# Kernel tuning notes

Hardware: AMD Instinct MI355X
Metric: run time of the kernel (lower is better)

The kernel has to match this reference:

```python
import jax, jax.numpy as jnp
import numpy as np

B, C_IN, L, NCLASS = 256, 6, 512, 10

def setup_inputs() -> dict:
    key = jax.random.key(0)
    ks = jax.random.split(key, 16)
    g = lambda k, shp, s=0.05: jax.random.normal(k, shp, dtype=jnp.float32) * s
    return {
        "x": jax.random.normal(ks[0], (B, C_IN, L), dtype=jnp.float32),
        "conv1_w": g(ks[1], (32, C_IN, 3)),
        "conv1_b": g(ks[2], (32,)),
        "bn1_g": jnp.ones((32,), jnp.float32),
        "bn1_b": jnp.zeros((32,), jnp.float32),
        "bn1_m": g(ks[3], (32,)),
        "bn1_v": jnp.abs(g(ks[4], (32,))) + 1.0,
        "conv2_w": g(ks[5], (64, 32, 3)),
        "conv2_b": g(ks[6], (64,)),
        "bn2_g": jnp.ones((64,), jnp.float32),
        "bn2_b": jnp.zeros((64,), jnp.float32),
        "bn2_m": g(ks[7], (64,)),
        "bn2_v": jnp.abs(g(ks[8], (64,))) + 1.0,
        "wq": g(ks[9], (64, 64)),
        "bq": g(ks[10], (64,)),
        "wk": g(ks[11], (64, 64)),
        "bk": g(ks[12], (64,)),
        "wv": g(ks[13], (64, 64)),
        "bv": g(ks[14], (64,)),
        "fc_w": g(ks[15], (NCLASS, 64)),
        "fc_b": jnp.zeros((NCLASS,), jnp.float32),
    }

def _conv1d(x, w, b):
    # x: [B, C, L], w: [O, C, 3], padding=1 -> same length
    y = jax.lax.conv_general_dilated(
        x, w, window_strides=(1,), padding=[(1, 1)],
        dimension_numbers=("NCH", "OIH", "NCH"))
    return y + b[None, :, None]

def _bn(x, g, b, m, v, eps=1e-5):
    # eval-mode BatchNorm1d over channel dim of [B, C, L]
    inv = g * jax.lax.rsqrt(v + eps)
    return x * inv[None, :, None] + (b - m * inv)[None, :, None]

def reference(x, conv1_w, conv1_b, bn1_g, bn1_b, bn1_m, bn1_v,
              conv2_w, conv2_b, bn2_g, bn2_b, bn2_m, bn2_v,
              wq, bq, wk, bk, wv, bv, fc_w, fc_b):
    h = jax.nn.relu(_bn(_conv1d(x, conv1_w, conv1_b), bn1_g, bn1_b, bn1_m, bn1_v))
    h = jax.nn.relu(_bn(_conv1d(h, conv2_w, conv2_b), bn2_g, bn2_b, bn2_m, bn2_v))
    h = h.transpose(0, 2, 1)                      # [B, L, 64]
    q = h @ wq.T + bq
    k = h @ wk.T + bk
    v = h @ wv.T + bv
    scores = jnp.einsum("bqd,bkd->bqk", q, k) / jnp.sqrt(jnp.float32(64.0))
    attn = jax.nn.softmax(scores, axis=-1)
    out = jnp.einsum("bqk,bkd->bqd", attn, v)     # [B, L, 64]
    pooled = out.mean(axis=1)                     # [B, 64]
    return pooled @ fc_w.T + fc_b                 # [B, n_class]
```

## Files before the change

kernel.cpp:

```cpp
#include <hip/hip_runtime.h>
#include <hip/hip_bf16.h>


#define NB 256
#define LL 512
#define CIN 6
#define NCLASS 10
#define SLAB 8192
#define QSC 0.18033688f

typedef __bf16 bf16x8 __attribute__((ext_vector_type(8)));
typedef float f32x4 __attribute__((ext_vector_type(4)));
typedef unsigned short us4 __attribute__((ext_vector_type(4)));
typedef unsigned short us8 __attribute__((ext_vector_type(8)));
typedef unsigned int u32x4 __attribute__((ext_vector_type(4)));

static __device__ __forceinline__ unsigned short f2b(float f) {
    __bf16 h = (__bf16)f;
    return __builtin_bit_cast(unsigned short, h);
}

__global__ __launch_bounds__(256) void prep_weights(
    const float* __restrict__ w1, const float* __restrict__ cb1,
    const float* __restrict__ g1, const float* __restrict__ be1,
    const float* __restrict__ m1, const float* __restrict__ v1,
    const float* __restrict__ w2, const float* __restrict__ cb2,
    const float* __restrict__ g2, const float* __restrict__ be2,
    const float* __restrict__ m2, const float* __restrict__ v2,
    const float* __restrict__ wq, const float* __restrict__ wk,
    const float* __restrict__ wv,
    unsigned short* __restrict__ w1p, float* __restrict__ b1f,
    unsigned short* __restrict__ w2p, float* __restrict__ b2f,
    unsigned short* __restrict__ wqp, unsigned short* __restrict__ wkp,
    unsigned short* __restrict__ wvp)
{
    const int tt = blockIdx.x * 256 + threadIdx.x;
    for (int idx = tt; idx < 1024; idx += 2048) {
        int c = idx >> 5, k = idx & 31;
        int dl = k >> 3, ci = k & 7;
        float inv = g1[c] * rsqrtf(v1[c] + 1e-5f);
        float val = (dl < 3 && ci < 6) ? w1[c * 18 + ci * 3 + dl] * inv : 0.f;
        w1p[idx] = f2b(val);
    }
    if (tt < 32) {
        float inv = g1[tt] * rsqrtf(v1[tt] + 1e-5f);
        b1f[tt] = be1[tt] + (cb1[tt] - m1[tt]) * inv;
    }
    for (int idx = tt; idx < 2048; idx += 2048) {
        int c2 = idx >> 5, ci = idx & 31;
        float inv = g2[c2] * rsqrtf(v2[c2] + 1e-5f);
        const float* wp = w2 + c2 * 96 + ci * 3;
        w2p[c2 * 96 +      ci] = f2b(wp[0] * inv);
        w2p[c2 * 96 + 32 + ci] = f2b(wp[1] * inv);
        w2p[c2 * 96 + 64 + ci] = f2b(wp[2] * inv);
    }
    if (tt >= 64 && tt < 128) {
        int c2 = tt - 64;
        float inv = g2[c2] * rsqrtf(v2[c2] + 1e-5f);
        b2f[c2] = be2[c2] + (cb2[c2] - m2[c2]) * inv;
    }
    for (int idx = tt; idx < 4096; idx += 2048) {
        int d = idx >> 6, k = idx & 63;
        int kc = k >> 5, quad = (k >> 3) & 3, e = k & 7;
        int ch = kc * 32 + (e >> 2) * 16 + quad * 4 + (e & 3);
        wqp[idx] = f2b(wq[d * 64 + ch] * QSC);
        wkp[idx] = f2b(wk[d * 64 + ch]);
        wvp[idx] = f2b(wv[d * 64 + ch]);
    }
}

__global__ __launch_bounds__(512, 2) void fused_all(
    const float* __restrict__ x,
    const unsigned short* __restrict__ w1p, const float* __restrict__ b1f,
    const unsigned short* __restrict__ w2p, const float* __restrict__ b2f,
    const unsigned short* __restrict__ wqp, const unsigned short* __restrict__ wkp,
    const unsigned short* __restrict__ wvp,
    const float* __restrict__ bq, const float* __restrict__ bk,
    const float* __restrict__ bvp,
    const float* __restrict__ fcw, const float* __restrict__ fcb,
    float* __restrict__ outp)
{
    const int b = blockIdx.x;
    const int t = threadIdx.x;
    const int w = t >> 6, lane = t & 63, quad = lane >> 4, lc = lane & 15;

    __shared__ __align__(16) char smem[16 * SLAB + 8192];
    unsigned short* xstage = (unsigned short*)(smem + 16 * SLAB);
    float* redw   = (float*)(smem + 16 * SLAB) + w * 64;
    float* pooled = (float*)(smem + 16 * SLAB + 4096);

    {
        us8 pk;
        #pragma unroll
        for (int ci = 0; ci < 6; ci++)
            pk[ci] = f2b(x[((size_t)b * CIN + ci) * LL + t]);
        pk[6] = 0; pk[7] = 0;
        *(us8*)&xstage[t * 8] = pk;
    }
    __syncthreads();

    bf16x8 aQ4[4][2];
    #pragma unroll
    for (int sg = 0; sg < 2; sg++) {
        const int g = 2 * w + sg;
        char* gslab = smem + g * SLAB;
        unsigned short* h1sl = (unsigned short*)gslab;
        unsigned short* Kf   = (unsigned short*)gslab;
        unsigned short* Vf   = (unsigned short*)(gslab + 4096);

        bf16x8 bW1[2];
        #pragma unroll
        for (int nt = 0; nt < 2; nt++)
            bW1[nt] = *(const bf16x8*)(w1p + (nt * 16 + lc) * 32 + quad * 8);
        f32x4 b1q[2];
        #pragma unroll
        for (int nt = 0; nt < 2; nt++)
            b1q[nt] = *(const f32x4*)&b1f[nt * 16 + quad * 4];
        #pragma unroll
        for (int mt = 0; mt < 3; mt++) {
            int j = mt * 16 + lc;
            int P = g * 32 - 1 + j;
            int src = P + quad - 1;
            bool okx = (src >= 0) && (src < LL);
            int srcc = src < 0 ? 0 : (src > 511 ? 511 : src);
            u32x4 xv = *(const u32x4*)&xstage[srcc * 8];
            if (!okx) { xv[0] = 0u; xv[1] = 0u; xv[2] = 0u; xv[3] = 0u; }
            bf16x8 aX = __builtin_bit_cast(bf16x8, xv);
            bool pv = (P >= 0) && (P < LL);
            #pragma unroll
            for (int nt = 0; nt < 2; nt++) {
                f32x4 z = {0.f, 0.f, 0.f, 0.f};
                f32x4 h = __builtin_amdgcn_mfma_f32_16x16x32_bf16(bW1[nt], aX, z, 0, 0, 0);
                us4 pk;
                #pragma unroll
                for (int r = 0; r < 4; r++) {
                    float y = h[r] + b1q[nt][r];
                    y = (pv && y > 0.f) ? y : 0.f;
                    pk[r] = f2b(y);
                }
                if (j < 34)
                    *(us4*)&h1sl[j * 40 + nt * 16 + quad * 4] = pk;
            }
        }

        bf16x8 bX[2][3], aW2[4][3];
        #pragma unroll
        for (int rt = 0; rt < 2; rt++)
            #pragma unroll
            for (int kc = 0; kc < 3; kc++)
                bX[rt][kc] = *(const bf16x8*)&h1sl[(rt * 16 + lc + kc) * 40 + quad * 8];
        #pragma unroll
        for (int nt = 0; nt < 4; nt++)
            #pragma unroll
            for (int kc = 0; kc < 3; kc++)
                aW2[nt][kc] = *(const bf16x8*)(w2p + (nt * 16 + lc) * 96 + kc * 32 + quad * 8);

        f32x4 acc2[4][2];
        #pragma unroll
        for (int nt = 0; nt < 4; nt++)
            #pragma unroll
            for (int rt = 0; rt < 2; rt++) {
                f32x4 a = {0.f, 0.f, 0.f, 0.f};
                a = __builtin_amdgcn_mfma_f32_16x16x32_bf16(aW2[nt][0], bX[rt][0], a, 0, 0, 0);
                a = __builtin_amdgcn_mfma_f32_16x16x32_bf16(aW2[nt][1], bX[rt][1], a, 0, 0, 0);
                acc2[nt][rt] = __builtin_amdgcn_mfma_f32_16x16x32_bf16(aW2[nt][2], bX[rt][2], a, 0, 0, 0);
            }

        bf16x8 aH[2][2];
        #pragma unroll
        for (int nt2 = 0; nt2 < 4; nt2++) {
            f32x4 bb2 = *(const f32x4*)&b2f[nt2 * 16 + quad * 4];
            #pragma unroll
            for (int rt = 0; rt < 2; rt++)
                #pragma unroll
                for (int reg = 0; reg < 4; reg++) {
                    float y = acc2[nt2][rt][reg] + bb2[reg];
                    aH[rt][nt2 >> 1][(nt2 & 1) * 4 + reg] = (__bf16)(y > 0.f ? y : 0.f);
                }
        }

        {
            f32x4 Cq[4][2], bbq[4];
            #pragma unroll
            for (int nt = 0; nt < 4; nt++) {
                bf16x8 aW0 = *(const bf16x8*)(wqp + (nt * 16 + lc) * 64 + quad * 8);
                bf16x8 aW1 = *(const bf16x8*)(wqp + (nt * 16 + lc) * 64 + 32 + quad * 8);
                bbq[nt] = *(const f32x4*)&bq[nt * 16 + quad * 4];
                #pragma unroll
                for (int rt = 0; rt < 2; rt++) {
                    f32x4 a = {0.f, 0.f, 0.f, 0.f};
                    a = __builtin_amdgcn_mfma_f32_16x16x32_bf16(aW0, aH[rt][0], a, 0, 0, 0);
                    Cq[nt][rt] = __builtin_amdgcn_mfma_f32_16x16x32_bf16(aW1, aH[rt][1], a, 0, 0, 0);
                }
            }
            #pragma unroll
            for (int rt = 0; rt < 2; rt++)
                #pragma unroll
                for (int nt = 0; nt < 4; nt++)
                    #pragma unroll
                    for (int reg = 0; reg < 4; reg++)
                        aQ4[sg * 2 + rt][nt >> 1][(nt & 1) * 4 + reg] =
                            (__bf16)(Cq[nt][rt][reg] + bbq[nt][reg] * QSC);
        }
        {
            f32x4 Ck[4][2], bbk[4];
            #pragma unroll
            for (int nt = 0; nt < 4; nt++) {
                bf16x8 aW0 = *(const bf16x8*)(wkp + (nt * 16 + lc) * 64 + quad * 8);
                bf16x8 aW1 = *(const bf16x8*)(wkp + (nt * 16 + lc) * 64 + 32 + quad * 8);
                bbk[nt] = *(const f32x4*)&bk[nt * 16 + quad * 4];
                #pragma unroll
                for (int rt = 0; rt < 2; rt++) {
                    f32x4 a = {0.f, 0.f, 0.f, 0.f};
                    a = __builtin_amdgcn_mfma_f32_16x16x32_bf16(aW0, aH[rt][0], a, 0, 0, 0);
                    Ck[nt][rt] = __builtin_amdgcn_mfma_f32_16x16x32_bf16(aW1, aH[rt][1], a, 0, 0, 0);
                }
            }
            #pragma unroll
            for (int rt = 0; rt < 2; rt++)
                #pragma unroll
                for (int kc = 0; kc < 2; kc++) {
                    us8 pk;
                    #pragma unroll
                    for (int e = 0; e < 8; e++) {
                        int nt = kc * 2 + (e >> 2), reg = e & 3;
                        pk[e] = f2b(Ck[nt][rt][reg] + bbk[nt][reg]);
                    }
                    *(us8*)&Kf[((rt * 2 + kc) << 9) + lane * 8] = pk;
                }
        }

        #pragma unroll
        for (int nt = 0; nt < 4; nt++) {
            bf16x8 bW0 = *(const bf16x8*)(wvp + (nt * 16 + lc) * 64 + quad * 8);
            bf16x8 bW1 = *(const bf16x8*)(wvp + (nt * 16 + lc) * 64 + 32 + quad * 8);
            const float bvv = bvp[nt * 16 + lc];
            f32x4 a0, a1;
            {
                f32x4 z = {0.f, 0.f, 0.f, 0.f};
                z = __builtin_amdgcn_mfma_f32_16x16x32_bf16(aH[0][0], bW0, z, 0, 0, 0);
                a0 = __builtin_amdgcn_mfma_f32_16x16x32_bf16(aH[0][1], bW1, z, 0, 0, 0);
            }
            {
                f32x4 z = {0.f, 0.f, 0.f, 0.f};
                z = __builtin_amdgcn_mfma_f32_16x16x32_bf16(aH[1][0], bW0, z, 0, 0, 0);
                a1 = __builtin_amdgcn_mfma_f32_16x16x32_bf16(aH[1][1], bW1, z, 0, 0, 0);
            }
            us8 pk;
            #pragma unroll
            for (int reg = 0; reg < 4; reg++) {
                pk[reg]     = f2b(a0[reg] + bvv);
                pk[4 + reg] = f2b(a1[reg] + bvv);
            }
            *(us8*)&Vf[nt * 512 + lane * 8] = pk;
        }
    }

    __syncthreads();

    f32x4 outacc[4][4];
    #pragma unroll
    for (int rt = 0; rt < 4; rt++)
        #pragma unroll
        for (int dt = 0; dt < 4; dt++) outacc[rt][dt] = (f32x4){0.f, 0.f, 0.f, 0.f};
    float den[4] = {0.f, 0.f, 0.f, 0.f};

    bf16x8 bK2[2][2];
    {
        const unsigned short* sK = (const unsigned short*)smem;
        #pragma unroll
        for (int nt = 0; nt < 2; nt++)
            #pragma unroll
            for (int kc = 0; kc < 2; kc++)
                bK2[nt][kc] = *(const bf16x8*)&sK[((nt * 2 + kc) << 9) + lane * 8];
    }
    f32x4 sv[2][4];
    #pragma unroll
    for (int nt = 0; nt < 2; nt++)
        #pragma unroll
        for (int rt = 0; rt < 4; rt++) {
            f32x4 z = {0.f, 0.f, 0.f, 0.f};
            z = __builtin_amdgcn_mfma_f32_16x16x32_bf16(bK2[nt][0], aQ4[rt][0], z, 0, 0, 0);
            sv[nt][rt] = __builtin_amdgcn_mfma_f32_16x16x32_bf16(bK2[nt][1], aQ4[rt][1], z, 0, 0, 0);
        }

    for (int cc = 0; cc < 16; cc++) {
        const unsigned short* sV = (const unsigned short*)(smem + cc * SLAB + 4096);
        bf16x8 bV[4];
        #pragma unroll
        for (int dt = 0; dt < 4; dt++)
            bV[dt] = *(const bf16x8*)&sV[dt * 512 + lane * 8];
        if (cc < 15) {
            const unsigned short* sKn = (const unsigned short*)(smem + (cc + 1) * SLAB);
            #pragma unroll
            for (int nt = 0; nt < 2; nt++)
                #pragma unroll
                for (int kc = 0; kc < 2; kc++)
                    bK2[nt][kc] = *(const bf16x8*)&sKn[((nt * 2 + kc) << 9) + lane * 8];
        }
        bf16x8 aP[4];
        #pragma unroll
        for (int rt = 0; rt < 4; rt++)
            #pragma unroll
            for (int nt = 0; nt < 2; nt++)
                #pragma unroll
                for (int reg = 0; reg < 4; reg++) {
                    float p = __builtin_amdgcn_exp2f(sv[nt][rt][reg]);
                    den[rt] += p;
                    aP[rt][nt * 4 + reg] = (__bf16)p;
                }
        __builtin_amdgcn_s_setprio(1);
        #pragma unroll
        for (int rt = 0; rt < 4; rt++)
            #pragma unroll
            for (int dt = 0; dt < 4; dt++)
                outacc[rt][dt] = __builtin_amdgcn_mfma_f32_16x16x32_bf16(aP[rt], bV[dt], outacc[rt][dt], 0, 0, 0);
        if (cc < 15) {
            #pragma unroll
            for (int nt = 0; nt < 2; nt++)
                #pragma unroll
                for (int rt = 0; rt < 4; rt++) {
                    f32x4 z = {0.f, 0.f, 0.f, 0.f};
                    z = __builtin_amdgcn_mfma_f32_16x16x32_bf16(bK2[nt][0], aQ4[rt][0], z, 0, 0, 0);
                    sv[nt][rt] = __builtin_amdgcn_mfma_f32_16x16x32_bf16(bK2[nt][1], aQ4[rt][1], z, 0, 0, 0);
                }
        }
        __builtin_amdgcn_s_setprio(0);
    }

    float rden[4][4];
    #pragma unroll
    for (int rt = 0; rt < 4; rt++) {
        float d2 = den[rt];
        d2 += __shfl_xor(d2, 16);
        d2 += __shfl_xor(d2, 32);
        d2 = 1.0f / d2;
        #pragma unroll
        for (int reg = 0; reg < 4; reg++)
            rden[rt][reg] = __shfl(d2, quad * 4 + reg);
    }
    #pragma unroll
    for (int dt = 0; dt < 4; dt++) {
        float ps = 0.f;
        #pragma unroll
        for (int rt = 0; rt < 4; rt++)
            #pragma unroll
            for (int reg = 0; reg < 4; reg++)
                ps += outacc[rt][dt][reg] * rden[rt][reg];
        ps += __shfl_xor(ps, 16);
        ps += __shfl_xor(ps, 32);
        if (quad == 0) redw[dt * 16 + lc] = ps;
    }
    __syncthreads();
    if (t < 64) {
        float s = 0.f;
        #pragma unroll
        for (int ww = 0; ww < 8; ww++)
            s += *(const float*)(smem + 16 * SLAB + ww * 256 + t * 4);
        pooled[t] = s * (1.0f / 512.0f);
    }
    __syncthreads();
    if (t < NCLASS) {
        float acc = fcb[t];
        #pragma unroll
        for (int d = 0; d < 64; d++) acc += pooled[d] * fcw[t * 64 + d];
        outp[b * NCLASS + t] = acc;
    }
}

extern "C" void kernel_launch(void* const* d_in, const int* in_sizes, int n_in,
                              void* d_out, int out_size, void* d_ws, size_t ws_size,
                              hipStream_t stream)
{
    const float* x   = (const float*)d_in[0];
    const float* w1  = (const float*)d_in[1];
    const float* cb1 = (const float*)d_in[2];
    const float* g1  = (const float*)d_in[3];
    const float* be1 = (const float*)d_in[4];
    const float* m1  = (const float*)d_in[5];
    const float* v1  = (const float*)d_in[6];
    const float* w2  = (const float*)d_in[7];
    const float* cb2 = (const float*)d_in[8];
    const float* g2  = (const float*)d_in[9];
    const float* be2 = (const float*)d_in[10];
    const float* m2  = (const float*)d_in[11];
    const float* v2  = (const float*)d_in[12];
    const float* wq  = (const float*)d_in[13];
    const float* bq  = (const float*)d_in[14];
    const float* wk  = (const float*)d_in[15];
    const float* bk  = (const float*)d_in[16];
    const float* wv  = (const float*)d_in[17];
    const float* bv  = (const float*)d_in[18];
    const float* fcw = (const float*)d_in[19];
    const float* fcb = (const float*)d_in[20];
    float* out = (float*)d_out;

    char* ws = (char*)d_ws;
    unsigned short* w1p = (unsigned short*)(ws);
    float*          b1f = (float*)(ws + 2048u);
    float*          b2f = (float*)(ws + 2176u);
    unsigned short* w2p = (unsigned short*)(ws + 2432u);
    unsigned short* wqp = (unsigned short*)(ws + 14720u);
    unsigned short* wkp = (unsigned short*)(ws + 22912u);
    unsigned short* wvp = (unsigned short*)(ws + 31104u);

    prep_weights<<<dim3(8), 256, 0, stream>>>(w1, cb1, g1, be1, m1, v1,
                                              w2, cb2, g2, be2, m2, v2,
                                              wq, wk, wv,
                                              w1p, b1f, w2p, b2f, wqp, wkp, wvp);
    fused_all<<<dim3(NB), 512, 0, stream>>>(x, w1p, b1f, w2p, b2f,
                                            wqp, wkp, wvp,
                                            bq, bk, bv, fcw, fcb, out);
}
```

Measured before the change: 124.2 us.

## Batch both slab groups per wave and compute softmax denominator via MFMA

Restructures the per-wave prologue so conv2 and the Q/K/V projections for both slab groups run in one pass, loading each weight fragment once and reusing it across both groups instead of reloading it per group. In the attention loop, the softmax denominator is now an extra MFMA against a vector of ones, replacing per-element float adds and the later cross-lane shuffle reduction. This moves VALU work onto the matrix unit but adds MFMA instructions, raises register pressure from the doubled live arrays, and sums the denominator over bf16-rounded probabilities instead of fp32 ones.

```diff
diff --git a/kernel.cpp b/kernel.cpp
--- a/kernel.cpp
+++ b/kernel.cpp
@@ -89,6 +89,9 @@
     float* redw   = (float*)(smem + 16 * SLAB) + w * 64;
     float* pooled = (float*)(smem + 16 * SLAB + 4096);
 
+    unsigned short* slab[2] = { (unsigned short*)(smem + (2 * w) * SLAB),
+                                (unsigned short*)(smem + (2 * w + 1) * SLAB) };
+
     {
         us8 pk;
         #pragma unroll
@@ -99,15 +102,7 @@
     }
     __syncthreads();
 
-    bf16x8 aQ4[4][2];
-    #pragma unroll
-    for (int sg = 0; sg < 2; sg++) {
-        const int g = 2 * w + sg;
-        char* gslab = smem + g * SLAB;
-        unsigned short* h1sl = (unsigned short*)gslab;
-        unsigned short* Kf   = (unsigned short*)gslab;
-        unsigned short* Vf   = (unsigned short*)(gslab + 4096);
-
+    {
         bf16x8 bW1[2];
         #pragma unroll
         for (int nt = 0; nt < 2; nt++)
@@ -117,134 +112,153 @@
         for (int nt = 0; nt < 2; nt++)
             b1q[nt] = *(const f32x4*)&b1f[nt * 16 + quad * 4];
         #pragma unroll
-        for (int mt = 0; mt < 3; mt++) {
-            int j = mt * 16 + lc;
-            int P = g * 32 - 1 + j;
-            int src = P + quad - 1;
-            bool okx = (src >= 0) && (src < LL);
-            int srcc = src < 0 ? 0 : (src > 511 ? 511 : src);
-            u32x4 xv = *(const u32x4*)&xstage[srcc * 8];
-            if (!okx) { xv[0] = 0u; xv[1] = 0u; xv[2] = 0u; xv[3] = 0u; }
-            bf16x8 aX = __builtin_bit_cast(bf16x8, xv);
-            bool pv = (P >= 0) && (P < LL);
-            #pragma unroll
-            for (int nt = 0; nt < 2; nt++) {
-                f32x4 z = {0.f, 0.f, 0.f, 0.f};
-                f32x4 h = __builtin_amdgcn_mfma_f32_16x16x32_bf16(bW1[nt], aX, z, 0, 0, 0);
-                us4 pk;
-                #pragma unroll
-                for (int r = 0; r < 4; r++) {
-                    float y = h[r] + b1q[nt][r];
-                    y = (pv && y > 0.f) ? y : 0.f;
-                    pk[r] = f2b(y);
+        for (int sg = 0; sg < 2; sg++) {
+            const int g = 2 * w + sg;
+            unsigned short* h1sl = slab[sg];
+            #pragma unroll
+            for (int mt = 0; mt < 3; mt++) {
+                int j = mt * 16 + lc;
+                int P = g * 32 - 1 + j;
+                int src = P + quad - 1;
+                bool okx = (src >= 0) && (src < LL);
+                int srcc = src < 0 ? 0 : (src > 511 ? 511 : src);
+                u32x4 xv = *(const u32x4*)&xstage[srcc * 8];
+                if (!okx) { xv[0] = 0u; xv[1] = 0u; xv[2] = 0u; xv[3] = 0u; }
+                bf16x8 aX = __builtin_bit_cast(bf16x8, xv);
+                bool pv = (P >= 0) && (P < LL);
+                #pragma unroll
+                for (int nt = 0; nt < 2; nt++) {
+                    f32x4 z = {0.f, 0.f, 0.f, 0.f};
+                    f32x4 h = __builtin_amdgcn_mfma_f32_16x16x32_bf16(bW1[nt], aX, z, 0, 0, 0);
+                    us4 pk;
+                    #pragma unroll
+                    for (int r = 0; r < 4; r++) {
+                        float y = h[r] + b1q[nt][r];
+                        y = (pv && y > 0.f) ? y : 0.f;
+                        pk[r] = f2b(y);
+                    }
+                    if (j < 34)
+                        *(us4*)&h1sl[j * 40 + nt * 16 + quad * 4] = pk;
                 }
-                if (j < 34)
-                    *(us4*)&h1sl[j * 40 + nt * 16 + quad * 4] = pk;
-            }
-        }
-
-        bf16x8 bX[2][3], aW2[4][3];
+            }
+        }
+    }
+
+    bf16x8 bX[2][2][3];
+    #pragma unroll
+    for (int sg = 0; sg < 2; sg++)
         #pragma unroll
         for (int rt = 0; rt < 2; rt++)
             #pragma unroll
             for (int kc = 0; kc < 3; kc++)
-                bX[rt][kc] = *(const bf16x8*)&h1sl[(rt * 16 + lc + kc) * 40 + quad * 8];
-        #pragma unroll
-        for (int nt = 0; nt < 4; nt++)
-            #pragma unroll
-            for (int kc = 0; kc < 3; kc++)
-                aW2[nt][kc] = *(const bf16x8*)(w2p + (nt * 16 + lc) * 96 + kc * 32 + quad * 8);
-
-        f32x4 acc2[4][2];
-        #pragma unroll
-        for (int nt = 0; nt < 4; nt++)
+                bX[sg][rt][kc] = *(const bf16x8*)&slab[sg][(rt * 16 + lc + kc) * 40 + quad * 8];
+
+    f32x4 acc2[2][4][2];
+    #pragma unroll
+    for (int nt = 0; nt < 4; nt++) {
+        bf16x8 aW0 = *(const bf16x8*)(w2p + (nt * 16 + lc) * 96 + quad * 8);
+        bf16x8 aW1 = *(const bf16x8*)(w2p + (nt * 16 + lc) * 96 + 32 + quad * 8);
+        bf16x8 aW2 = *(const bf16x8*)(w2p + (nt * 16 + lc) * 96 + 64 + quad * 8);
+        #pragma unroll
+        for (int sg = 0; sg < 2; sg++)
             #pragma unroll
             for (int rt = 0; rt < 2; rt++) {
                 f32x4 a = {0.f, 0.f, 0.f, 0.f};
-                a = __builtin_amdgcn_mfma_f32_16x16x32_bf16(aW2[nt][0], bX[rt][0], a, 0, 0, 0);
-                a = __builtin_amdgcn_mfma_f32_16x16x32_bf16(aW2[nt][1], bX[rt][1], a, 0, 0, 0);
-                acc2[nt][rt] = __builtin_amdgcn_mfma_f32_16x16x32_bf16(aW2[nt][2], bX[rt][2], a, 0, 0, 0);
-            }
-
-        bf16x8 aH[2][2];
-        #pragma unroll
-        for (int nt2 = 0; nt2 < 4; nt2++) {
-            f32x4 bb2 = *(const f32x4*)&b2f[nt2 * 16 + quad * 4];
+                a = __builtin_amdgcn_mfma_f32_16x16x32_bf16(aW0, bX[sg][rt][0], a, 0, 0, 0);
+                a = __builtin_amdgcn_mfma_f32_16x16x32_bf16(aW1, bX[sg][rt][1], a, 0, 0, 0);
+                acc2[sg][nt][rt] = __builtin_amdgcn_mfma_f32_16x16x32_bf16(aW2, bX[sg][rt][2], a, 0, 0, 0);
+            }
+    }
+
+    bf16x8 aH[2][2][2];
+    #pragma unroll
+    for (int nt2 = 0; nt2 < 4; nt2++) {
+        f32x4 bb2 = *(const f32x4*)&b2f[nt2 * 16 + quad * 4];
+        #pragma unroll
+        for (int sg = 0; sg < 2; sg++)
             #pragma unroll
             for (int rt = 0; rt < 2; rt++)
                 #pragma unroll
                 for (int reg = 0; reg < 4; reg++) {
-                    float y = acc2[nt2][rt][reg] + bb2[reg];
-                    aH[rt][nt2 >> 1][(nt2 & 1) * 4 + reg] = (__bf16)(y > 0.f ? y : 0.f);
+                    float y = acc2[sg][nt2][rt][reg] + bb2[reg];
+                    aH[sg][rt][nt2 >> 1][(nt2 & 1) * 4 + reg] = (__bf16)(y > 0.f ? y : 0.f);
                 }
-        }
-
-        {
-            f32x4 Cq[4][2], bbq[4];
-            #pragma unroll
-            for (int nt = 0; nt < 4; nt++) {
-                bf16x8 aW0 = *(const bf16x8*)(wqp + (nt * 16 + lc) * 64 + quad * 8);
-                bf16x8 aW1 = *(const bf16x8*)(wqp + (nt * 16 + lc) * 64 + 32 + quad * 8);
-                bbq[nt] = *(const f32x4*)&bq[nt * 16 + quad * 4];
+    }
+
+    f32x4 bbq[4], bbk[4];
+    #pragma unroll
+    for (int nt = 0; nt < 4; nt++) {
+        bbq[nt] = *(const f32x4*)&bq[nt * 16 + quad * 4];
+        bbk[nt] = *(const f32x4*)&bk[nt * 16 + quad * 4];
+    }
+
+    bf16x8 aQ4[4][2];
+    #pragma unroll
+    for (int nt = 0; nt < 4; nt++) {
+        bf16x8 aW0 = *(const bf16x8*)(wqp + (nt * 16 + lc) * 64 + quad * 8);
+        bf16x8 aW1 = *(const bf16x8*)(wqp + (nt * 16 + lc) * 64 + 32 + quad * 8);
+        #pragma unroll
+        for (int sg = 0; sg < 2; sg++)
+            #pragma unroll
+            for (int rt = 0; rt < 2; rt++) {
+                f32x4 a = {0.f, 0.f, 0.f, 0.f};
+                a = __builtin_amdgcn_mfma_f32_16x16x32_bf16(aW0, aH[sg][rt][0], a, 0, 0, 0);
+                a = __builtin_amdgcn_mfma_f32_16x16x32_bf16(aW1, aH[sg][rt][1], a, 0, 0, 0);
+                #pragma unroll
+                for (int reg = 0; reg < 4; reg++)
+                    aQ4[sg * 2 + rt][nt >> 1][(nt & 1) * 4 + reg] =
+                        (__bf16)(a[reg] + bbq[nt][reg] * QSC);
+            }
+    }
+
+    #pragma unroll
+    for (int kc = 0; kc < 2; kc++) {
+        f32x4 Ck[2][2][2];
+        #pragma unroll
+        for (int j = 0; j < 2; j++) {
+            int nt = kc * 2 + j;
+            bf16x8 aW0 = *(const bf16x8*)(wkp + (nt * 16 + lc) * 64 + quad * 8);
+            bf16x8 aW1 = *(const bf16x8*)(wkp + (nt * 16 + lc) * 64 + 32 + quad * 8);
+            #pragma unroll
+            for (int sg = 0; sg < 2; sg++)
                 #pragma unroll
                 for (int rt = 0; rt < 2; rt++) {
                     f32x4 a = {0.f, 0.f, 0.f, 0.f};
-                    a = __builtin_amdgcn_mfma_f32_16x16x32_bf16(aW0, aH[rt][0], a, 0, 0, 0);
-                    Cq[nt][rt] = __builtin_amdgcn_mfma_f32_16x16x32_bf16(aW1, aH[rt][1], a, 0, 0, 0);
+                    a = __builtin_amdgcn_mfma_f32_16x16x32_bf16(aW0, aH[sg][rt][0], a, 0, 0, 0);
+                    Ck[j][sg][rt] = __builtin_amdgcn_mfma_f32_16x16x32_bf16(aW1, aH[sg][rt][1], a, 0, 0, 0);
                 }
-            }
-            #pragma unroll
-            for (int rt = 0; rt < 2; rt++)
-                #pragma unroll
-                for (int nt = 0; nt < 4; nt++)
-                    #pragma unroll
-                    for (int reg = 0; reg < 4; reg++)
-                        aQ4[sg * 2 + rt][nt >> 1][(nt & 1) * 4 + reg] =
-                            (__bf16)(Cq[nt][rt][reg] + bbq[nt][reg] * QSC);
-        }
-        {
-            f32x4 Ck[4][2], bbk[4];
-            #pragma unroll
-            for (int nt = 0; nt < 4; nt++) {
-                bf16x8 aW0 = *(const bf16x8*)(wkp + (nt * 16 + lc) * 64 + quad * 8);
-                bf16x8 aW1 = *(const bf16x8*)(wkp + (nt * 16 + lc) * 64 + 32 + quad * 8);
-                bbk[nt] = *(const f32x4*)&bk[nt * 16 + quad * 4];
-                #pragma unroll
-                for (int rt = 0; rt < 2; rt++) {
-                    f32x4 a = {0.f, 0.f, 0.f, 0.f};
-                    a = __builtin_amdgcn_mfma_f32_16x16x32_bf16(aW0, aH[rt][0], a, 0, 0, 0);
-                    Ck[nt][rt] = __builtin_amdgcn_mfma_f32_16x16x32_bf16(aW1, aH[rt][1], a, 0, 0, 0);
+        }
+        #pragma unroll
+        for (int sg = 0; sg < 2; sg++)
+            #pragma unroll
+            for (int rt = 0; rt < 2; rt++) {
+                us8 pk;
+                #pragma unroll
+                for (int e = 0; e < 8; e++) {
+                    int j = e >> 2, reg = e & 3, nt = kc * 2 + j;
+                    pk[e] = f2b(Ck[j][sg][rt][reg] + bbk[nt][reg]);
                 }
-            }
-            #pragma unroll
-            for (int rt = 0; rt < 2; rt++)
-                #pragma unroll
-                for (int kc = 0; kc < 2; kc++) {
-                    us8 pk;
-                    #pragma unroll
-                    for (int e = 0; e < 8; e++) {
-                        int nt = kc * 2 + (e >> 2), reg = e & 3;
-                        pk[e] = f2b(Ck[nt][rt][reg] + bbk[nt][reg]);
-                    }
-                    *(us8*)&Kf[((rt * 2 + kc) << 9) + lane * 8] = pk;
-                }
-        }
-
-        #pragma unroll
-        for (int nt = 0; nt < 4; nt++) {
-            bf16x8 bW0 = *(const bf16x8*)(wvp + (nt * 16 + lc) * 64 + quad * 8);
-            bf16x8 bW1 = *(const bf16x8*)(wvp + (nt * 16 + lc) * 64 + 32 + quad * 8);
-            const float bvv = bvp[nt * 16 + lc];
+                *(us8*)&slab[sg][((rt * 2 + kc) << 9) + lane * 8] = pk;
+            }
+    }
+
+    #pragma unroll
+    for (int nt = 0; nt < 4; nt++) {
+        bf16x8 bW0 = *(const bf16x8*)(wvp + (nt * 16 + lc) * 64 + quad * 8);
+        bf16x8 bW1 = *(const bf16x8*)(wvp + (nt * 16 + lc) * 64 + 32 + quad * 8);
+        const float bvv = bvp[nt * 16 + lc];
+        #pragma unroll
+        for (int sg = 0; sg < 2; sg++) {
             f32x4 a0, a1;
             {
                 f32x4 z = {0.f, 0.f, 0.f, 0.f};
-                z = __builtin_amdgcn_mfma_f32_16x16x32_bf16(aH[0][0], bW0, z, 0, 0, 0);
-                a0 = __builtin_amdgcn_mfma_f32_16x16x32_bf16(aH[0][1], bW1, z, 0, 0, 0);
+                z = __builtin_amdgcn_mfma_f32_16x16x32_bf16(aH[sg][0][0], bW0, z, 0, 0, 0);
+                a0 = __builtin_amdgcn_mfma_f32_16x16x32_bf16(aH[sg][0][1], bW1, z, 0, 0, 0);
             }
             {
                 f32x4 z = {0.f, 0.f, 0.f, 0.f};
-                z = __builtin_amdgcn_mfma_f32_16x16x32_bf16(aH[1][0], bW0, z, 0, 0, 0);
-                a1 = __builtin_amdgcn_mfma_f32_16x16x32_bf16(aH[1][1], bW1, z, 0, 0, 0);
+                z = __builtin_amdgcn_mfma_f32_16x16x32_bf16(aH[sg][1][0], bW0, z, 0, 0, 0);
+                a1 = __builtin_amdgcn_mfma_f32_16x16x32_bf16(aH[sg][1][1], bW1, z, 0, 0, 0);
             }
             us8 pk;
             #pragma unroll
@@ -252,7 +266,7 @@
                 pk[reg]     = f2b(a0[reg] + bvv);
                 pk[4 + reg] = f2b(a1[reg] + bvv);
             }
-            *(us8*)&Vf[nt * 512 + lane * 8] = pk;
+            *(us8*)&slab[sg][2048 + nt * 512 + lane * 8] = pk;
         }
     }
 
@@ -263,7 +277,12 @@
     for (int rt = 0; rt < 4; rt++)
         #pragma unroll
         for (int dt = 0; dt < 4; dt++) outacc[rt][dt] = (f32x4){0.f, 0.f, 0.f, 0.f};
-    float den[4] = {0.f, 0.f, 0.f, 0.f};
+    f32x4 accDen[4];
+    #pragma unroll
+    for (int rt = 0; rt < 4; rt++) accDen[rt] = (f32x4){0.f, 0.f, 0.f, 0.f};
+    bf16x8 bOne;
+    #pragma unroll
+    for (int e = 0; e < 8; e++) bOne[e] = (__bf16)1.0f;
 
     bf16x8 bK2[2][2];
     {
@@ -304,17 +323,16 @@
             #pragma unroll
             for (int nt = 0; nt < 2; nt++)
                 #pragma unroll
-                for (int reg = 0; reg < 4; reg++) {
-                    float p = __builtin_amdgcn_exp2f(sv[nt][rt][reg]);
-                    den[rt] += p;
-                    aP[rt][nt * 4 + reg] = (__bf16)p;
-                }
+                for (int reg = 0; reg < 4; reg++)
+                    aP[rt][nt * 4 + reg] = (__bf16)__builtin_amdgcn_exp2f(sv[nt][rt][reg]);
         __builtin_amdgcn_s_setprio(1);
         #pragma unroll
-        for (int rt = 0; rt < 4; rt++)
+        for (int rt = 0; rt < 4; rt++) {
             #pragma unroll
             for (int dt = 0; dt < 4; dt++)
                 outacc[rt][dt] = __builtin_amdgcn_mfma_f32_16x16x32_bf16(aP[rt], bV[dt], outacc[rt][dt], 0, 0, 0);
+            accDen[rt] = __builtin_amdgcn_mfma_f32_16x16x32_bf16(aP[rt], bOne, accDen[rt], 0, 0, 0);
+        }
         if (cc < 15) {
             #pragma unroll
             for (int nt = 0; nt < 2; nt++)
@@ -330,15 +348,10 @@
 
     float rden[4][4];
     #pragma unroll
-    for (int rt = 0; rt < 4; rt++) {
-        float d2 = den[rt];
-        d2 += __shfl_xor(d2, 16);
-        d2 += __shfl_xor(d2, 32);
-        d2 = 1.0f / d2;
+    for (int rt = 0; rt < 4; rt++)
         #pragma unroll
         for (int reg = 0; reg < 4; reg++)
-            rden[rt][reg] = __shfl(d2, quad * 4 + reg);
-    }
+            rden[rt][reg] = 1.0f / accDen[rt][reg];
     #pragma unroll
     for (int dt = 0; dt < 4; dt++) {
         float ps = 0.f;
```

Result: faster. 119.9 us (-3.5%).
